# Kernel optimization log

Measured on AMD Instinct MI355X. Metric: run time of the kernel, lower is better.

Reference implementation:

```python
import jax, jax.numpy as jnp
import numpy as np
from jax import lax

EPS = 1e-5  # BatchNorm eps (torch default)


def _bn_relu_conv3x3_s2(x, bn_w, bn_b, bn_m, bn_v, w, b):
    # eval-mode BatchNorm2d -> ReLU -> conv3x3 stride 2 pad 1 (NCHW)
    inv = bn_w / jnp.sqrt(bn_v + EPS)
    y = x * inv[None, :, None, None] + (bn_b - bn_m * inv)[None, :, None, None]
    y = jax.nn.relu(y)
    y = lax.conv_general_dilated(y, w, window_strides=(2, 2),
                                 padding=((1, 1), (1, 1)),
                                 dimension_numbers=("NCHW", "OIHW", "NCHW"))
    return y + b[None, :, None, None]


def _avgpool2x2(x):
    B, C, H, W = x.shape
    return x.reshape(B, C, H // 2, 2, W // 2, 2).mean(axis=(3, 5))


def setup_inputs() -> dict:
    key = jax.random.key(0)
    ks = jax.random.split(key, 24)
    C, C3 = 128, 128 // 3
    d = {"x": jax.random.normal(ks[0], (8, C, 96, 96), jnp.float32)}
    for i, p in enumerate(["f", "g", "h"]):
        base = 1 + i * 6
        d[p + "_bn_w"] = jax.random.uniform(ks[base], (C,), jnp.float32, 0.5, 1.5)
        d[p + "_bn_b"] = jax.random.normal(ks[base + 1], (C,), jnp.float32) * 0.1
        d[p + "_bn_m"] = jax.random.normal(ks[base + 2], (C,), jnp.float32) * 0.1
        d[p + "_bn_v"] = jax.random.uniform(ks[base + 3], (C,), jnp.float32, 0.5, 1.5)
        d[p + "_w"] = jax.random.normal(ks[base + 4], (C, C, 3, 3), jnp.float32) * (1.0 / np.sqrt(9 * C))
        d[p + "_b"] = jax.random.normal(ks[base + 5], (C,), jnp.float32) * 0.01
    d["se_cw"] = jax.random.normal(ks[19], (C3, 2 * C), jnp.float32) * (1.0 / np.sqrt(2 * C))
    d["se_cb"] = jax.random.normal(ks[20], (C3,), jnp.float32) * 0.01
    d["se_uw"] = jax.random.normal(ks[21], (C, C3), jnp.float32) * (1.0 / np.sqrt(C3))
    d["se_ub"] = jax.random.normal(ks[22], (C,), jnp.float32) * 0.01
    d["gamma"] = jax.random.normal(ks[23], (1,), jnp.float32) * 0.5
    return d


def reference(x, f_bn_w, f_bn_b, f_bn_m, f_bn_v, f_w, f_b,
              g_bn_w, g_bn_b, g_bn_m, g_bn_v, g_w, g_b,
              h_bn_w, h_bn_b, h_bn_m, h_bn_v, h_w, h_b,
              se_cw, se_cb, se_uw, se_ub, gamma):
    B, C, H, W = x.shape
    left = _avgpool2x2(x)  # isPrimary=False branch -> [B,C,H/2,W/2]

    f = _bn_relu_conv3x3_s2(x, f_bn_w, f_bn_b, f_bn_m, f_bn_v, f_w, f_b)
    g = _bn_relu_conv3x3_s2(x, g_bn_w, g_bn_b, g_bn_m, g_bn_v, g_w, g_b)
    h = _bn_relu_conv3x3_s2(x, h_bn_w, h_bn_b, h_bn_m, h_bn_v, h_w, h_b)

    Ho, Wo = f.shape[2], f.shape[3]
    N = Ho * Wo
    ff = f.reshape(B, C, N)
    gg = g.reshape(B, C, N)
    hh = h.reshape(B, C, N)

    # s = softmax over last axis of f^T g : [B, N, N]
    scores = jnp.einsum("bcn,bcm->bnm", ff, gg)
    attn = jax.nn.softmax(scores, axis=2)
    s = jnp.einsum("bcn,bnm->bcm", hh, attn).reshape(B, C, Ho, Wo)
    s = gamma[0] * s

    # CompetitiveSE: global-avg x and s -> concat(2C) -> ReLU/1x1(C//3) -> ReLU/1x1(C)
    wx = x.mean(axis=(2, 3))          # [B, C]
    ws = s.mean(axis=(2, 3))          # [B, C]
    wcat = jnp.concatenate([wx, ws], axis=1)  # [B, 2C]
    se = jax.nn.relu(wcat) @ se_cw.T + se_cb
    se = jax.nn.relu(se) @ se_uw.T + se_ub    # [B, C]

    return (left + s) * (1.0 + se[:, :, None, None])
```

## Files before the change

### kernel.cpp

```cpp
#include <hip/hip_runtime.h>
#include <hip/hip_bf16.h>

#define B_   8
#define C_   128
#define H_   96
#define W_   96
#define HP_  98
#define HO_  48
#define N_   2304
#define K_CONV 1152
#define PLANE_IN  9216
#define TOT_OUT (B_*C_*N_)
#define LOG2E 1.4426950408889634f

typedef __attribute__((ext_vector_type(8))) short          s16x8;
typedef __attribute__((ext_vector_type(8))) unsigned short u16x8;
typedef __attribute__((ext_vector_type(4))) unsigned short u16x4;
typedef __attribute__((ext_vector_type(4))) float          f32x4;

#define SW(row, q)   (((row) << 6) + ((((q) ^ (((row) >> 1) & 3))) << 4))
#define SW8(row, q)  (((row) << 7) + ((((q) ^ ((row) & 7))) << 4))
#define SW16(row, q) (((row) << 8) + ((((q) ^ ((row) & 15))) << 4))

__device__ __forceinline__ float fexp2(float x) { return __builtin_amdgcn_exp2f(x); }
__device__ __forceinline__ float flog2(float x) { return __builtin_amdgcn_logf(x); }

__device__ __forceinline__ ushort f2bf(float f) {
  __hip_bfloat16 h = __float2bfloat16(f);
  return *reinterpret_cast<ushort*>(&h);
}

__device__ __forceinline__ float block_reduce_sum_256(float v) {
  #pragma unroll
  for (int o = 32; o > 0; o >>= 1) v += __shfl_down(v, o, 64);
  __shared__ float r[4];
  int lane = threadIdx.x & 63, wv = threadIdx.x >> 6;
  if (lane == 0) r[wv] = v;
  __syncthreads();
  float s = 0.f;
  if (threadIdx.x == 0) s = r[0] + r[1] + r[2] + r[3];
  __syncthreads();
  return s;
}

__global__ __launch_bounds__(256) void k_prep_w(
    const float* __restrict__ w0, const float* __restrict__ w1, const float* __restrict__ w2,
    ushort* __restrict__ o0, ushort* __restrict__ o1, ushort* __restrict__ o2,
    const float* __restrict__ bw0, const float* __restrict__ bb0,
    const float* __restrict__ bm0, const float* __restrict__ bv0,
    const float* __restrict__ bw1, const float* __restrict__ bb1,
    const float* __restrict__ bm1, const float* __restrict__ bv1,
    const float* __restrict__ bw2, const float* __restrict__ bb2,
    const float* __restrict__ bm2, const float* __restrict__ bv2,
    float* __restrict__ pinv, float* __restrict__ pbeta) {
  int p = blockIdx.y;
  if (blockIdx.x == (C_ * K_CONV) / 256) {
    if (p == 0 && threadIdx.x < 128) {
      int c = threadIdx.x;
      const float* ws[3] = {bw0, bw1, bw2};
      const float* bs[3] = {bb0, bb1, bb2};
      const float* ms[3] = {bm0, bm1, bm2};
      const float* vs[3] = {bv0, bv1, bv2};
      #pragma unroll
      for (int pb = 0; pb < 3; ++pb) {
        float iv = ws[pb][c] / sqrtf(vs[pb][c] + 1e-5f);
        pinv[pb * 128 + c] = iv;
        pbeta[pb * 128 + c] = bs[pb][c] - ms[pb][c] * iv;
      }
    }
    return;
  }
  const float* w = (p == 0 ? w0 : p == 1 ? w1 : w2);
  ushort* wb = (p == 0 ? o0 : p == 1 ? o1 : o2);
  int id = blockIdx.x * 256 + threadIdx.x;
  int co = id / K_CONV, rem = id - co * K_CONV;
  int tap = rem >> 7, ci = rem & 127;
  wb[id] = f2bf(w[co * K_CONV + ci * 9 + tap]);
}

__global__ __launch_bounds__(256) void k_prep_y(const float* __restrict__ x,
                                                const float* __restrict__ pinv,
                                                const float* __restrict__ pbeta,
                                                ushort* __restrict__ y0,
                                                ushort* __restrict__ y1,
                                                ushort* __restrict__ y2,
                                                float* __restrict__ wcat) {
  const int h1 = blockIdx.x, b = blockIdx.y, t = threadIdx.x;
  ushort* ys[3] = {y0 + (size_t)b * HP_ * HP_ * C_,
                   y1 + (size_t)b * HP_ * HP_ * C_,
                   y2 + (size_t)b * HP_ * HP_ * C_};
  u16x8 zer = (u16x8)0;
  if (h1 == 0 || h1 == HP_ - 1) {
    for (int p = 0; p < 3; ++p)
      for (int g = t; g < HP_ * C_ / 8; g += 256)
        *(u16x8*)(ys[p] + (size_t)h1 * HP_ * C_ + g * 8) = zer;
    return;
  }
  __shared__ float xs[128][97];
  const int h = h1 - 1;
  const float* xb = x + (size_t)b * C_ * PLANE_IN + h * W_;
  for (int id = t; id < 128 * 24; id += 256) {
    int ci = id / 24, w4 = id - ci * 24;
    float4 v = *(const float4*)(xb + (size_t)ci * PLANE_IN + w4 * 4);
    xs[ci][w4 * 4 + 0] = v.x; xs[ci][w4 * 4 + 1] = v.y;
    xs[ci][w4 * 4 + 2] = v.z; xs[ci][w4 * 4 + 3] = v.w;
  }
  __syncthreads();
  if (t < 128) {
    float s = 0.f;
    #pragma unroll
    for (int k = 0; k < 96; ++k) s += xs[t][k];
    atomicAdd(&wcat[b * 256 + t], s);
  }
  if (t >= 128 && t < 160) {
    int tt = t - 128;
    int side = tt >> 4, cg = tt & 15;
    for (int p = 0; p < 3; ++p)
      *(u16x8*)(ys[p] + ((size_t)h1 * HP_ + (side ? HP_ - 1 : 0)) * C_ + cg * 8) = zer;
  }
  for (int p = 0; p < 3; ++p) {
    const float* inv = pinv + p * 128;
    const float* bet = pbeta + p * 128;
    for (int g = t; g < 96 * 16; g += 256) {
      int wdx = g >> 4, cg = g & 15;
      u16x8 o;
      #pragma unroll
      for (int k = 0; k < 8; ++k) {
        int ci = cg * 8 + k;
        o[k] = f2bf(fmaxf(xs[ci][wdx] * inv[ci] + bet[ci], 0.f));
      }
      *(u16x8*)(ys[p] + ((size_t)h1 * HP_ + (wdx + 1)) * C_ + cg * 8) = o;
    }
  }
}

__global__ __launch_bounds__(256) void k_conv3(
    const ushort* __restrict__ y0, const ushort* __restrict__ y1, const ushort* __restrict__ y2,
    const ushort* __restrict__ w0, const ushort* __restrict__ w1, const ushort* __restrict__ w2,
    const float* __restrict__ bi0, const float* __restrict__ bi1, const float* __restrict__ bi2,
    const float* __restrict__ gammap,
    ushort* __restrict__ fo, ushort* __restrict__ go, ushort* __restrict__ ho) {
  __shared__ __align__(16) char smem[24576];
  const int br = blockIdx.y, b = blockIdx.z, n0 = blockIdx.x * 64;
  const int t = threadIdx.x, l = t & 63, w = t >> 6;
  const ushort* yb = (br == 0 ? y0 : br == 1 ? y1 : y2) + (size_t)b * HP_ * HP_ * C_;
  const ushort* wb = (br == 0 ? w0 : br == 1 ? w1 : w2);
  const float* bias = (br == 0 ? bi0 : br == 1 ? bi1 : bi2);
  const float gm = (br == 2) ? gammap[0] : (br == 0 ? LOG2E : 1.f);
  const int pos = t >> 2, q = t & 3;
  const int n_glob = n0 + pos;
  const int oh = n_glob / HO_, ow = n_glob - oh * HO_;
  const int mh = (w & 1) * 64, nh = (w >> 1) * 32;
  f32x4 acc[4][2];
  #pragma unroll
  for (int i = 0; i < 4; ++i)
    #pragma unroll
    for (int j = 0; j < 2; ++j) acc[i][j] = (f32x4)0.f;

  u16x8 sA0, sA1, sB;
  auto LD = [&](int k0) {
    int tap = k0 >> 7, ci0 = k0 & 127;
    int kh = tap / 3, kw = tap - kh * 3;
    sA0 = *(const u16x8*)(wb + (t >> 2) * K_CONV + k0 + (t & 3) * 8);
    sA1 = *(const u16x8*)(wb + ((t >> 2) + 64) * K_CONV + k0 + (t & 3) * 8);
    int h1 = 2 * oh + kh, w1 = 2 * ow + kw;
    sB = *(const u16x8*)(yb + ((size_t)h1 * HP_ + w1) * C_ + ci0 + q * 8);
  };
  auto ST = [&](char* As, char* Bs) {
    *(u16x8*)(As + SW(t >> 2, t & 3)) = sA0;
    *(u16x8*)(As + SW((t >> 2) + 64, t & 3)) = sA1;
    *(u16x8*)(Bs + SW(pos, q)) = sB;
  };

  LD(0);
  ST(smem, smem + 16384);
  __syncthreads();
  for (int s = 0; s < 36; ++s) {
    char* Asc = smem + ((s & 1) << 13);
    char* Bsc = smem + 16384 + ((s & 1) << 12);
    if (s < 35) LD((s + 1) * 32);
    s16x8 af[4], bf[2];
    #pragma unroll
    for (int i = 0; i < 4; ++i) {
      int r = mh + i * 16 + (l & 15);
      af[i] = *(const s16x8*)(Asc + SW(r, (l >> 4)));
    }
    #pragma unroll
    for (int j = 0; j < 2; ++j) {
      int r = nh + j * 16 + (l & 15);
      bf[j] = *(const s16x8*)(Bsc + SW(r, (l >> 4)));
    }
    __builtin_amdgcn_s_setprio(1);
    #pragma unroll
    for (int i = 0; i < 4; ++i)
      #pragma unroll
      for (int j = 0; j < 2; ++j)
        acc[i][j] = __builtin_amdgcn_mfma_f32_16x16x32_bf16(af[i], bf[j], acc[i][j], 0, 0, 0);
    __builtin_amdgcn_s_setprio(0);
    if (s < 35)
      ST(smem + (((s + 1) & 1) << 13), smem + 16384 + (((s + 1) & 1) << 12));
    __syncthreads();
  }

  if (br < 2) {
    ushort* out = (br == 0) ? fo : go;
    ushort* tb = (ushort*)smem;
    #pragma unroll
    for (int i = 0; i < 4; ++i) {
      int co4 = mh + i * 16 + (l >> 4) * 4;
      float4 bi = *(const float4*)&bias[co4];
      float bia[4] = {bi.x, bi.y, bi.z, bi.w};
      #pragma unroll
      for (int j = 0; j < 2; ++j) {
        int pp = nh + j * 16 + (l & 15);
        #pragma unroll
        for (int r = 0; r < 4; ++r)
          tb[pp * 128 + co4 + r] = f2bf((acc[i][j][r] + bia[r]) * gm);
      }
    }
    __syncthreads();
    #pragma unroll
    for (int it = 0; it < 4; ++it) {
      int g = t + it * 256;
      int row = g >> 4, gg = g & 15;
      u16x8 d = *(const u16x8*)(tb + row * 128 + gg * 8);
      *(u16x8*)(out + ((size_t)b * N_ + n0 + row) * C_ + gg * 8) = d;
    }
  } else {
    ushort* tb = (ushort*)smem;
    #pragma unroll
    for (int i = 0; i < 4; ++i) {
      int co4 = mh + i * 16 + (l >> 4) * 4;
      float4 bi = *(const float4*)&bias[co4];
      float bia[4] = {bi.x, bi.y, bi.z, bi.w};
      #pragma unroll
      for (int j = 0; j < 2; ++j) {
        int pp = nh + j * 16 + (l & 15);
        #pragma unroll
        for (int r = 0; r < 4; ++r)
          tb[(co4 + r) * 64 + pp] = f2bf((acc[i][j][r] + bia[r]) * gm);
      }
    }
    __syncthreads();
    for (int g = t; g < 1024; g += 256) {
      int co = g >> 3, off2 = (g & 7) * 8;
      u16x8 d = *(const u16x8*)(tb + co * 64 + off2);
      *(u16x8*)(ho + ((size_t)b * C_ + co) * N_ + n0 + off2) = d;
    }
  }
}

__global__ __launch_bounds__(256) void k_stats(const ushort* __restrict__ f,
                                               const ushort* __restrict__ g,
                                               float2* __restrict__ pstats) {
  __shared__ __align__(16) char smem[32768];
  const int blk = blockIdx.x;
  const int b = blk & 7, t2 = blk >> 3;
  const int n0 = (t2 % 36) * 64, mz = t2 / 36;
  const int t = threadIdx.x, l = t & 63, w = t >> 6, lo = l & 15, quad = l >> 4;
  const ushort* fb = f + (size_t)b * N_ * C_;
  const ushort* gb = g + (size_t)b * N_ * C_;
  s16x8 af[4];
  #pragma unroll
  for (int ks = 0; ks < 4; ++ks)
    af[ks] = *(const s16x8*)(fb + (size_t)(n0 + w * 16 + lo) * C_ + (ks * 4 + quad) * 8);
  float mloc[4], lloc[4];
  #pragma unroll
  for (int r = 0; r < 4; ++r) { mloc[r] = -1e30f; lloc[r] = 0.f; }
  const int m_beg = mz * 576;

  u16x8 st[4];
  #pragma unroll
  for (int it = 0; it < 4; ++it) {
    int G = t + it * 256, row = G >> 4, g16 = G & 15;
    st[it] = *(const u16x8*)(gb + (size_t)(m_beg + row) * C_ + g16 * 8);
  }
  #pragma unroll
  for (int it = 0; it < 4; ++it) {
    int G = t + it * 256, row = G >> 4, g16 = G & 15;
    *(u16x8*)(smem + SW16(row, g16)) = st[it];
  }
  __syncthreads();

  #pragma unroll
  for (int i9 = 0; i9 < 9; ++i9) {
    char* gs = smem + ((i9 & 1) << 14);
    if (i9 < 8) {
      int m0n = m_beg + (i9 + 1) * 64;
      #pragma unroll
      for (int it = 0; it < 4; ++it) {
        int G = t + it * 256, row = G >> 4, g16 = G & 15;
        st[it] = *(const u16x8*)(gb + (size_t)(m0n + row) * C_ + g16 * 8);
      }
    }
    f32x4 acc[4];
    #pragma unroll
    for (int j = 0; j < 4; ++j) acc[j] = (f32x4)0.f;
    __builtin_amdgcn_s_setprio(1);
    #pragma unroll
    for (int ks = 0; ks < 4; ++ks)
      #pragma unroll
      for (int j = 0; j < 4; ++j) {
        s16x8 bf = *(const s16x8*)(gs + SW16(j * 16 + lo, ks * 4 + quad));
        acc[j] = __builtin_amdgcn_mfma_f32_16x16x32_bf16(af[ks], bf, acc[j], 0, 0, 0);
      }
    __builtin_amdgcn_s_setprio(0);
    #pragma unroll
    for (int r = 0; r < 4; ++r) {
      float vmax = fmaxf(fmaxf(acc[0][r], acc[1][r]), fmaxf(acc[2][r], acc[3][r]));
      float mn = fmaxf(mloc[r], vmax);
      lloc[r] = lloc[r] * fexp2(mloc[r] - mn) +
                fexp2(acc[0][r] - mn) + fexp2(acc[1][r] - mn) +
                fexp2(acc[2][r] - mn) + fexp2(acc[3][r] - mn);
      mloc[r] = mn;
    }
    if (i9 < 8) {
      char* gn = smem + (((i9 + 1) & 1) << 14);
      #pragma unroll
      for (int it = 0; it < 4; ++it) {
        int G = t + it * 256, row = G >> 4, g16 = G & 15;
        *(u16x8*)(gn + SW16(row, g16)) = st[it];
      }
    }
    __syncthreads();
  }
  #pragma unroll
  for (int r = 0; r < 4; ++r) {
    #pragma unroll
    for (int o = 1; o < 16; o <<= 1) {
      float mo = __shfl_xor(mloc[r], o, 64);
      float lo2 = __shfl_xor(lloc[r], o, 64);
      float mn = fmaxf(mloc[r], mo);
      lloc[r] = lloc[r] * fexp2(mloc[r] - mn) + lo2 * fexp2(mo - mn);
      mloc[r] = mn;
    }
  }
  if (lo == 0) {
    #pragma unroll
    for (int r = 0; r < 4; ++r)
      pstats[((size_t)mz * B_ + b) * N_ + n0 + w * 16 + quad * 4 + r] =
          make_float2(mloc[r], lloc[r]);
  }
}

__global__ __launch_bounds__(256) void k_stats_red(const float2* __restrict__ p,
                                                   float* __restrict__ astat) {
  int idx = blockIdx.x * 256 + threadIdx.x;
  if (idx >= B_ * N_) return;
  float mx = -1e30f, ls = 0.f;
  #pragma unroll
  for (int z = 0; z < 4; ++z) {
    float2 s = p[(size_t)z * B_ * N_ + idx];
    float mn = fmaxf(mx, s.x);
    ls = ls * fexp2(mx - mn) + s.y * fexp2(s.x - mn);
    mx = mn;
  }
  astat[idx] = -mx - flog2(ls);
}

__global__ __launch_bounds__(256) void k_attn_out(const ushort* __restrict__ f,
                                                  const ushort* __restrict__ g,
                                                  const ushort* __restrict__ h,
                                                  const float* __restrict__ astat,
                                                  float* __restrict__ spart) {
  __shared__ __align__(16) char smem[32768];
  char* gs = smem;
  char* pTb = smem + 16384;
  const int blk = blockIdx.x;
  const int b = blk & 7, t2 = blk >> 3;
  const int m0 = (t2 % 36) * 64, nz = t2 / 36;
  const int t = threadIdx.x, l = t & 63, w = t >> 6, lo = l & 15, quad = l >> 4;
  const ushort* fb = f + (size_t)b * N_ * C_;
  const ushort* gb = g + (size_t)b * N_ * C_;
  const ushort* hb = h + (size_t)b * C_ * N_;
  const float* ab = astat + (size_t)b * N_;
  #pragma unroll
  for (int it = 0; it < 4; ++it) {
    int G = t + it * 256, row = G >> 4, g16 = G & 15;
    *(u16x8*)(gs + SW16(row, g16)) = *(const u16x8*)(gb + (size_t)(m0 + row) * C_ + g16 * 8);
  }
  f32x4 accs[2][4];
  #pragma unroll
  for (int i = 0; i < 2; ++i)
    #pragma unroll
    for (int j = 0; j < 4; ++j) accs[i][j] = (f32x4)0.f;
  const int n_beg = nz * 576;

  s16x8 af[2][4];
  s16x8 ahc[2][2];
  float ax[2][4];

  auto LOAD_AF = [&](int i, int p) {
    int nb = n_beg + i * 64;
    #pragma unroll
    for (int ks = 0; ks < 4; ++ks)
      af[p][ks] = *(const s16x8*)(fb + (size_t)(nb + w * 16 + lo) * C_ + (ks * 4 + quad) * 8);
    float4 av = *(const float4*)(ab + nb + w * 16 + quad * 4);
    ax[p][0] = av.x; ax[p][1] = av.y; ax[p][2] = av.z; ax[p][3] = av.w;
  };
  auto LOAD_AH = [&](int i) {
    int nb = n_beg + i * 64;
    #pragma unroll
    for (int ii = 0; ii < 2; ++ii)
      #pragma unroll
      for (int ks = 0; ks < 2; ++ks)
        ahc[ii][ks] = *(const s16x8*)(hb + (size_t)((2 * w + ii) * 16 + lo) * N_ + nb + (ks * 4 + quad) * 8);
  };
  auto QKEXP = [&](int p) {
    char* pT = pTb + (p << 13);
    f32x4 sc[4];
    #pragma unroll
    for (int j = 0; j < 4; ++j) sc[j] = (f32x4)0.f;
    __builtin_amdgcn_s_setprio(1);
    #pragma unroll
    for (int ks = 0; ks < 4; ++ks)
      #pragma unroll
      for (int j = 0; j < 4; ++j) {
        s16x8 bg = *(const s16x8*)(gs + SW16(j * 16 + lo, ks * 4 + quad));
        sc[j] = __builtin_amdgcn_mfma_f32_16x16x32_bf16(af[p][ks], bg, sc[j], 0, 0, 0);
      }
    __builtin_amdgcn_s_setprio(0);
    const int nl = w * 16 + quad * 4;
    #pragma unroll
    for (int j = 0; j < 4; ++j) {
      u16x4 pv;
      #pragma unroll
      for (int r = 0; r < 4; ++r)
        pv[r] = f2bf(fexp2(sc[j][r] + ax[p][r]));
      *(u16x4*)(pT + SW8(j * 16 + lo, nl >> 3) + (nl & 7) * 2) = pv;
    }
  };
  auto PV = [&](int p) {
    char* pT = pTb + (p << 13);
    __builtin_amdgcn_s_setprio(1);
    #pragma unroll
    for (int ks = 0; ks < 2; ++ks)
      #pragma unroll
      for (int j = 0; j < 4; ++j) {
        s16x8 bp = *(const s16x8*)(pT + SW8(j * 16 + lo, ks * 4 + quad));
        accs[0][j] = __builtin_amdgcn_mfma_f32_16x16x32_bf16(ahc[0][ks], bp, accs[0][j], 0, 0, 0);
        accs[1][j] = __builtin_amdgcn_mfma_f32_16x16x32_bf16(ahc[1][ks], bp, accs[1][j], 0, 0, 0);
      }
    __builtin_amdgcn_s_setprio(0);
  };

  LOAD_AF(0, 0);
  LOAD_AH(0);
  __syncthreads();
  QKEXP(0);
  LOAD_AF(1, 1);
  #pragma unroll
  for (int i9 = 0; i9 < 9; ++i9) {
    __syncthreads();
    PV(i9 & 1);
    if (i9 < 8) {
      LOAD_AH(i9 + 1);
      QKEXP((i9 + 1) & 1);
      if (i9 < 7) LOAD_AF(i9 + 2, i9 & 1);
    }
  }
  float* outp = spart + (size_t)nz * TOT_OUT + (size_t)b * C_ * N_ + m0;
  float* ss = (float*)smem;
  #pragma unroll
  for (int ch = 0; ch < 2; ++ch) {
    __syncthreads();
    {
      int ci0 = w * 16 + quad * 4;
      #pragma unroll
      for (int j = 0; j < 4; ++j) {
        int m = j * 16 + lo;
        #pragma unroll
        for (int r = 0; r < 4; ++r)
          ss[(ci0 + r) * 68 + m] = accs[ch][j][r];
      }
    }
    __syncthreads();
    #pragma unroll
    for (int it = 0; it < 4; ++it) {
      int idx = t + it * 256;
      int ci = idx >> 4, mq = idx & 15;
      int c = (ci >> 4) * 32 + ch * 16 + (ci & 15);
      float4 v = *(const float4*)&ss[ci * 68 + mq * 4];
      *(float4*)&outp[(size_t)c * N_ + mq * 4] = v;
    }
  }
}

__global__ __launch_bounds__(256) void k_sred(const float* __restrict__ spart,
                                              float* __restrict__ sbuf,
                                              float* __restrict__ wcat) {
  int idx = blockIdx.x * 256 + threadIdx.x;
  float s = spart[idx] + spart[(size_t)TOT_OUT + idx] +
            spart[2 * (size_t)TOT_OUT + idx] + spart[3 * (size_t)TOT_OUT + idx];
  sbuf[idx] = s;
  float sm = block_reduce_sum_256(s);
  if (threadIdx.x == 0) {
    int bc = idx / N_;
    atomicAdd(&wcat[(bc >> 7) * 256 + 128 + (bc & 127)], sm);
  }
}

__global__ __launch_bounds__(128) void k_se(const float* __restrict__ wcat,
                                            const float* __restrict__ cw,
                                            const float* __restrict__ cb,
                                            const float* __restrict__ uw,
                                            const float* __restrict__ ub,
                                            float* __restrict__ se) {
  const int b = blockIdx.x, t = threadIdx.x;
  __shared__ float wc[256];
  __shared__ float s1[42];
  wc[t] = fmaxf(wcat[b * 256 + t] * (1.f / PLANE_IN), 0.f);
  wc[128 + t] = fmaxf(wcat[b * 256 + 128 + t] * (1.f / N_), 0.f);
  __syncthreads();
  if (t < 42) {
    float a = cb[t];
    const float* r = cw + (size_t)t * 256;
    for (int k = 0; k < 256; ++k) a += wc[k] * r[k];
    s1[t] = fmaxf(a, 0.f);
  }
  __syncthreads();
  {
    float a = ub[t];
    const float* r = uw + (size_t)t * 42;
    for (int j = 0; j < 42; ++j) a += s1[j] * r[j];
    se[b * 128 + t] = a;
  }
}

__global__ __launch_bounds__(256) void k_final(const float* __restrict__ x,
                                               const float* __restrict__ s,
                                               const float* __restrict__ se,
                                               float* __restrict__ out) {
  int idx = blockIdx.x * 256 + threadIdx.x;
  if (idx >= TOT_OUT) return;
  int m  = idx % N_;
  int bc = idx / N_;
  int oh = m / HO_, ow = m - oh * HO_;
  const float* xp = x + (size_t)bc * PLANE_IN;
  int ih = oh * 2, iw = ow * 2;
  float l = 0.25f * (xp[ih * W_ + iw] + xp[ih * W_ + iw + 1] +
                     xp[(ih + 1) * W_ + iw] + xp[(ih + 1) * W_ + iw + 1]);
  out[idx] = (l + s[idx]) * (1.f + se[bc]);
}

extern "C" void kernel_launch(void* const* d_in, const int* in_sizes, int n_in,
                              void* d_out, int out_size, void* d_ws, size_t ws_size,
                              hipStream_t stream) {
  (void)in_sizes; (void)n_in; (void)out_size; (void)ws_size;
  const float* x    = (const float*)d_in[0];
  const float* bnw[3] = {(const float*)d_in[1],  (const float*)d_in[7],  (const float*)d_in[13]};
  const float* bnb[3] = {(const float*)d_in[2],  (const float*)d_in[8],  (const float*)d_in[14]};
  const float* bnm[3] = {(const float*)d_in[3],  (const float*)d_in[9],  (const float*)d_in[15]};
  const float* bnv[3] = {(const float*)d_in[4],  (const float*)d_in[10], (const float*)d_in[16]};
  const float* cw_[3] = {(const float*)d_in[5],  (const float*)d_in[11], (const float*)d_in[17]};
  const float* cbb[3] = {(const float*)d_in[6],  (const float*)d_in[12], (const float*)d_in[18]};
  const float* secw = (const float*)d_in[19];
  const float* secb = (const float*)d_in[20];
  const float* seuw = (const float*)d_in[21];
  const float* seub = (const float*)d_in[22];
  const float* gamma = (const float*)d_in[23];
  float* out = (float*)d_out;

  char* ws = (char*)d_ws;
  size_t off = 0;
  auto alloc = [&](size_t bytes) -> char* {
    char* p = ws + off;
    off = (off + bytes + 255) & ~(size_t)255;
    return p;
  };
  ushort* yp[3];
  for (int p = 0; p < 3; ++p) yp[p] = (ushort*)alloc((size_t)B_ * HP_ * HP_ * C_ * 2);
  ushort* wb[3];
  for (int p = 0; p < 3; ++p) wb[p] = (ushort*)alloc((size_t)C_ * K_CONV * 2);
  ushort* fbuf = (ushort*)alloc((size_t)B_ * N_ * C_ * 2);
  ushort* gbuf = (ushort*)alloc((size_t)B_ * N_ * C_ * 2);
  ushort* hbuf = (ushort*)alloc((size_t)B_ * C_ * N_ * 2);
  float2* pstats = (float2*)alloc((size_t)4 * B_ * N_ * 8);
  float*  astat  = (float*)alloc((size_t)B_ * N_ * 4);
  float*  spart = (float*)alloc((size_t)4 * TOT_OUT * 4);
  float*  sbuf = (float*)alloc((size_t)TOT_OUT * 4);
  float*  wcat = (float*)alloc(B_ * 256 * 4);
  float*  sebuf = (float*)alloc(B_ * 128 * 4);
  float*  pinv  = (float*)alloc(3 * 128 * 4);
  float*  pbeta = (float*)alloc(3 * 128 * 4);

  hipMemsetAsync(wcat, 0, B_ * 256 * 4, stream);

  k_prep_w<<<dim3((C_ * K_CONV) / 256 + 1, 3), 256, 0, stream>>>(
      cw_[0], cw_[1], cw_[2], wb[0], wb[1], wb[2],
      bnw[0], bnb[0], bnm[0], bnv[0],
      bnw[1], bnb[1], bnm[1], bnv[1],
      bnw[2], bnb[2], bnm[2], bnv[2], pinv, pbeta);
  k_prep_y<<<dim3(HP_, B_), 256, 0, stream>>>(x, pinv, pbeta, yp[0], yp[1], yp[2], wcat);

  k_conv3<<<dim3(N_ / 64, 3, B_), 256, 0, stream>>>(yp[0], yp[1], yp[2],
                                                    wb[0], wb[1], wb[2],
                                                    cbb[0], cbb[1], cbb[2], gamma,
                                                    fbuf, gbuf, hbuf);

  k_stats<<<1152, 256, 0, stream>>>(fbuf, gbuf, pstats);
  k_stats_red<<<(B_ * N_ + 255) / 256, 256, 0, stream>>>(pstats, astat);
  k_attn_out<<<1152, 256, 0, stream>>>(fbuf, gbuf, hbuf, astat, spart);
  k_sred<<<TOT_OUT / 256, 256, 0, stream>>>(spart, sbuf, wcat);

  k_se<<<B_, 128, 0, stream>>>(wcat, secw, secb, seuw, seub, sebuf);

  k_final<<<(TOT_OUT + 255) / 256, 256, 0, stream>>>(x, sbuf, sebuf, out);
}
```

Before: 276.5 us.

## Fuse split-K partial reduction into final kernel and SE sums into attention

Drops the separate k_sred pass. The per-channel sums that feed the SE average are now computed in k_attn_out from its accumulators, using shuffle reductions and atomics. The four split partials are summed directly in k_final, which also handles two outputs per thread with vectorised loads. This removes one full write and read of the s buffer and one launch, at the cost of more atomics in the attention kernel and reading four partial buffers in the final pass.

After: 265.3 us. -4.0%, faster.

```diff
diff --git a/kernel.cpp b/kernel.cpp
--- a/kernel.cpp
+++ b/kernel.cpp
@@ -28,19 +28,6 @@
 __device__ __forceinline__ ushort f2bf(float f) {
   __hip_bfloat16 h = __float2bfloat16(f);
   return *reinterpret_cast<ushort*>(&h);
-}
-
-__device__ __forceinline__ float block_reduce_sum_256(float v) {
-  #pragma unroll
-  for (int o = 32; o > 0; o >>= 1) v += __shfl_down(v, o, 64);
-  __shared__ float r[4];
-  int lane = threadIdx.x & 63, wv = threadIdx.x >> 6;
-  if (lane == 0) r[wv] = v;
-  __syncthreads();
-  float s = 0.f;
-  if (threadIdx.x == 0) s = r[0] + r[1] + r[2] + r[3];
-  __syncthreads();
-  return s;
 }
 
 __global__ __launch_bounds__(256) void k_prep_w(
@@ -362,7 +349,8 @@
                                                   const ushort* __restrict__ g,
                                                   const ushort* __restrict__ h,
                                                   const float* __restrict__ astat,
-                                                  float* __restrict__ spart) {
+                                                  float* __restrict__ spart,
+                                                  float* __restrict__ wcat) {
   __shared__ __align__(16) char smem[32768];
   char* gs = smem;
   char* pTb = smem + 16384;
@@ -459,6 +447,19 @@
       if (i9 < 7) LOAD_AF(i9 + 2, i9 & 1);
     }
   }
+  #pragma unroll
+  for (int i = 0; i < 2; ++i) {
+    #pragma unroll
+    for (int r = 0; r < 4; ++r) {
+      float sm = accs[i][0][r] + accs[i][1][r] + accs[i][2][r] + accs[i][3][r];
+      #pragma unroll
+      for (int o = 1; o < 16; o <<= 1) sm += __shfl_xor(sm, o, 64);
+      if (lo == 0) {
+        int c = (2 * w + i) * 16 + quad * 4 + r;
+        atomicAdd(&wcat[(b << 8) + 128 + c], sm);
+      }
+    }
+  }
   float* outp = spart + (size_t)nz * TOT_OUT + (size_t)b * C_ * N_ + m0;
   float* ss = (float*)smem;
   #pragma unroll
@@ -483,20 +484,6 @@
       float4 v = *(const float4*)&ss[ci * 68 + mq * 4];
       *(float4*)&outp[(size_t)c * N_ + mq * 4] = v;
     }
-  }
-}
-
-__global__ __launch_bounds__(256) void k_sred(const float* __restrict__ spart,
-                                              float* __restrict__ sbuf,
-                                              float* __restrict__ wcat) {
-  int idx = blockIdx.x * 256 + threadIdx.x;
-  float s = spart[idx] + spart[(size_t)TOT_OUT + idx] +
-            spart[2 * (size_t)TOT_OUT + idx] + spart[3 * (size_t)TOT_OUT + idx];
-  sbuf[idx] = s;
-  float sm = block_reduce_sum_256(s);
-  if (threadIdx.x == 0) {
-    int bc = idx / N_;
-    atomicAdd(&wcat[(bc >> 7) * 256 + 128 + (bc & 127)], sm);
   }
 }
 
@@ -528,19 +515,30 @@
 }
 
 __global__ __launch_bounds__(256) void k_final(const float* __restrict__ x,
-                                               const float* __restrict__ s,
+                                               const float* __restrict__ spart,
                                                const float* __restrict__ se,
                                                float* __restrict__ out) {
   int idx = blockIdx.x * 256 + threadIdx.x;
-  if (idx >= TOT_OUT) return;
-  int m  = idx % N_;
-  int bc = idx / N_;
-  int oh = m / HO_, ow = m - oh * HO_;
+  if (idx >= TOT_OUT / 2) return;
+  int m2 = idx % (N_ / 2);
+  int bc = idx / (N_ / 2);
+  int oh = m2 / (HO_ / 2), owp = m2 - oh * (HO_ / 2);
+  size_t base = (size_t)bc * N_ + oh * HO_ + owp * 2;
   const float* xp = x + (size_t)bc * PLANE_IN;
-  int ih = oh * 2, iw = ow * 2;
-  float l = 0.25f * (xp[ih * W_ + iw] + xp[ih * W_ + iw + 1] +
-                     xp[(ih + 1) * W_ + iw] + xp[(ih + 1) * W_ + iw + 1]);
-  out[idx] = (l + s[idx]) * (1.f + se[bc]);
+  int ih = oh * 2, iw = owp * 4;
+  float4 a = *(const float4*)(xp + ih * W_ + iw);
+  float4 bb = *(const float4*)(xp + (ih + 1) * W_ + iw);
+  float l0 = 0.25f * (a.x + a.y + bb.x + bb.y);
+  float l1 = 0.25f * (a.z + a.w + bb.z + bb.w);
+  float2 s0 = *(const float2*)(spart + base);
+  float2 s1 = *(const float2*)(spart + (size_t)TOT_OUT + base);
+  float2 s2 = *(const float2*)(spart + 2 * (size_t)TOT_OUT + base);
+  float2 s3 = *(const float2*)(spart + 3 * (size_t)TOT_OUT + base);
+  float sc = 1.f + se[bc];
+  float2 o;
+  o.x = (l0 + s0.x + s1.x + s2.x + s3.x) * sc;
+  o.y = (l1 + s0.y + s1.y + s2.y + s3.y) * sc;
+  *(float2*)(out + base) = o;
 }
 
 extern "C" void kernel_launch(void* const* d_in, const int* in_sizes, int n_in,
@@ -578,7 +576,6 @@
   float2* pstats = (float2*)alloc((size_t)4 * B_ * N_ * 8);
   float*  astat  = (float*)alloc((size_t)B_ * N_ * 4);
   float*  spart = (float*)alloc((size_t)4 * TOT_OUT * 4);
-  float*  sbuf = (float*)alloc((size_t)TOT_OUT * 4);
   float*  wcat = (float*)alloc(B_ * 256 * 4);
   float*  sebuf = (float*)alloc(B_ * 128 * 4);
   float*  pinv  = (float*)alloc(3 * 128 * 4);
@@ -600,10 +597,9 @@
 
   k_stats<<<1152, 256, 0, stream>>>(fbuf, gbuf, pstats);
   k_stats_red<<<(B_ * N_ + 255) / 256, 256, 0, stream>>>(pstats, astat);
-  k_attn_out<<<1152, 256, 0, stream>>>(fbuf, gbuf, hbuf, astat, spart);
-  k_sred<<<TOT_OUT / 256, 256, 0, stream>>>(spart, sbuf, wcat);
+  k_attn_out<<<1152, 256, 0, stream>>>(fbuf, gbuf, hbuf, astat, spart, wcat);
 
   k_se<<<B_, 128, 0, stream>>>(wcat, secw, secb, seuw, seub, sebuf);
 
-  k_final<<<(TOT_OUT + 255) / 256, 256, 0, stream>>>(x, sbuf, sebuf, out);
-}
+  k_final<<<(TOT_OUT / 2 + 255) / 256, 256, 0, stream>>>(x, spart, sebuf, out);
+}
```
